# Kernel tuning notes

Hardware: AMD Instinct MI355X
Metric: run time of the kernel (lower is better)

## Reference

```python
import jax, jax.numpy as jnp
import numpy as np

DT = 0.01
T, B, I, H, O = 512, 128, 256, 1024, 256


def setup_inputs() -> dict:
    key = jax.random.key(0)
    ks = jax.random.split(key, 9)
    def xavier(k, out_f, in_f):
        lim = np.sqrt(6.0 / (in_f + out_f)).astype(np.float32)
        return jax.random.uniform(k, (out_f, in_f), jnp.float32, -lim, lim)
    return {
        "x": jax.random.normal(ks[0], (T, B, I), jnp.float32),
        "W_h": xavier(ks[1], H, I + H),                      # HRCell linear, no bias
        "gain": jnp.ones((H,), jnp.float32),
        "omega": jax.random.uniform(ks[2], (H,), jnp.float32, 10.0, 50.0),
        "b_offset": jax.random.uniform(ks[3], (H,), jnp.float32, 1.0, 6.0),
        "W_o": xavier(ks[4], H, H),                          # LICell linear, no bias
        "tau_mem": 20.0 + 5.0 * jax.random.normal(ks[5], (H,), jnp.float32),
        "W_out": xavier(ks[6], O, H),                        # readout Linear
        "b_out": jnp.zeros((O,), jnp.float32),
    }


def reference(x, W_h, gain, omega, b_offset, W_o, tau_mem, W_out, b_out):
    om = jnp.abs(omega)
    om2 = om * om
    b = om2 * 0.005 + jnp.abs(b_offset)          # damping coefficient per unit
    alpha = jnp.exp(-1.0 / jnp.abs(tau_mem))     # leaky-integrator decay
    Bsz = x.shape[1]
    Hd = W_h.shape[0]
    Od = W_out.shape[0]

    def step(carry, x_t):
        hu, hv, ou, acc = carry
        # HRCell: linear on concat(input, hidden_u), then harmonic update
        in_sum = jnp.concatenate([x_t, hu], axis=1) @ W_h.T   # [B, H]
        hv = hv + hu * DT
        hu = hu + in_sum * DT - b * hu * (2.0 * DT) - om2 * hv * DT
        hu = hu * gain                                        # normalize=False path
        # LICell: leaky integrator on projected hidden
        ou = ou * alpha + (hu @ W_o.T) * (1.0 - alpha)
        # readout, summed over time
        acc = acc + ou @ W_out.T + b_out
        return (hu, hv, ou, acc), None

    z = jnp.zeros((Bsz, Hd), x.dtype)
    init = (z, z, z, jnp.zeros((Bsz, Od), x.dtype))
    (hu, hv, ou, acc), _ = jax.lax.scan(step, init, x)
    return acc
```

## Files before the change

### kernel.cpp

```cpp
#include <hip/hip_runtime.h>
#include <math.h>

#define DT 0.01f
constexpr int T = 512, B = 128, I = 256, H = 1024, O = 256;
constexpr int K = I + H;

constexpr size_t OFF_OSUM  = 0;
constexpr size_t OFF_HUH0  = OFF_OSUM + (size_t)B * H;
constexpr size_t OFF_HUL0  = OFF_HUH0 + (size_t)B * H / 2;
constexpr size_t OFF_HUH1  = OFF_HUL0 + (size_t)B * H / 2;
constexpr size_t OFF_HUL1  = OFF_HUH1 + (size_t)B * H / 2;
constexpr size_t OFF_COEF  = OFF_HUL1 + (size_t)B * H / 2;
constexpr size_t OFF_FLAGS = OFF_COEF + 5 * (size_t)H;
constexpr size_t OFF_WHH   = OFF_FLAGS + 8192;
constexpr size_t OFF_WHL   = OFF_WHH + 64 * 40 * 64 * 8 / 2;
constexpr size_t OFF_WOH   = OFF_WHL + 64 * 40 * 64 * 8 / 2;
constexpr size_t OFF_WOL   = OFF_WOH + 64 * 32 * 64 * 8 / 2;

constexpr int SM_WHH  = 0;
constexpr int SM_WHL  = 65536;
constexpr int SM_REDS = 131072;
constexpr int SM_REDP = 139520;
constexpr int SM_BYTES = 147968;

typedef __attribute__((ext_vector_type(8))) short short8v;
typedef __attribute__((ext_vector_type(4))) float f32x4;

static __device__ inline short f2bf(float f) {
    unsigned u = __builtin_bit_cast(unsigned, f);
    u += 0x7fffu + ((u >> 16) & 1u);
    return (short)(u >> 16);
}
static __device__ inline float bf2f(short s) {
    return __builtin_bit_cast(float, ((unsigned)(unsigned short)s) << 16);
}

__global__ __launch_bounds__(256)
void init_kernel(float* __restrict__ ws, const float* __restrict__ omega,
                 const float* __restrict__ b_offset, const float* __restrict__ tau_mem,
                 const float* __restrict__ gain) {
    size_t tid = (size_t)blockIdx.x * blockDim.x + threadIdx.x;
    size_t stride = (size_t)gridDim.x * blockDim.x;
    for (size_t i = tid; i < (size_t)B * H; i += stride) ws[OFF_HUH0 + i] = 0.0f;
    for (size_t i = tid; i < 8192; i += stride) ws[OFF_FLAGS + i] = 0.0f;
    if (tid < H) {
        float om  = fabsf(omega[tid]);
        float om2 = om * om;
        float bb  = om2 * 0.005f + fabsf(b_offset[tid]);
        float al  = expf(-1.0f / fabsf(tau_mem[tid]));
        float g   = gain[tid];
        ws[OFF_COEF + 0 * H + tid] = g * (1.0f - 2.0f * bb * DT);
        ws[OFF_COEF + 1 * H + tid] = g * DT;
        ws[OFF_COEF + 2 * H + tid] = g * om2 * DT;
        ws[OFF_COEF + 3 * H + tid] = al;
        ws[OFF_COEF + 4 * H + tid] = 1.0f - al;
    }
}

template <int NKS, int KD>
__global__ __launch_bounds__(256)
void convert_kernel(const float* __restrict__ W, short* __restrict__ WH,
                    short* __restrict__ WL) {
    int g = blockIdx.x * 256 + threadIdx.x;
    int lane = g & 63;
    int ks = (g >> 6) % NKS;
    int cg = g / (NKS * 64);
    int col = cg * 16 + (lane & 15);
    int k = ks * 32 + ((lane >> 4) << 3);
    const float* src = W + (size_t)col * KD + k;
    short8v hi, lo;
    #pragma unroll
    for (int j = 0; j < 8; ++j) {
        float v = src[j];
        short h = f2bf(v);
        hi[j] = h;
        lo[j] = f2bf(v - bf2f(h));
    }
    *(short8v*)(WH + (size_t)g * 8) = hi;
    *(short8v*)(WL + (size_t)g * 8) = lo;
}

__global__ __launch_bounds__(512)
void rnn_persist(const float* __restrict__ x, float* __restrict__ ws) {
    extern __shared__ char sm[];
    float* redS = (float*)(sm + SM_REDS);
    float* redP = (float*)(sm + SM_REDP);
    __shared__ int role_sm;

    const float* coef = ws + OFF_COEF;
    float* osum_g = ws + OFF_OSUM;
    const short* huhS[2] = {(const short*)(ws + OFF_HUH0), (const short*)(ws + OFF_HUH1)};
    const short* hulS[2] = {(const short*)(ws + OFF_HUL0), (const short*)(ws + OFF_HUL1)};
    unsigned int* huhW[2] = {(unsigned int*)(ws + OFF_HUH0), (unsigned int*)(ws + OFF_HUH1)};
    unsigned int* hulW[2] = {(unsigned int*)(ws + OFF_HUL0), (unsigned int*)(ws + OFF_HUL1)};
    int* flags = (int*)(ws + OFF_FLAGS);
    int* ctr   = flags + 4096;

    const int tid = threadIdx.x;

    if (tid == 0) {
        unsigned xcc_;
        asm volatile("s_getreg_b32 %0, hwreg(HW_REG_XCC_ID)" : "=s"(xcc_));
        int slot = atomicAdd(ctr + (xcc_ & 7), 1);
        role_sm = (int)((xcc_ & 7) * 32 + (slot & 31));
    }
    __syncthreads();
    const int role = role_sm;
    const int xcc = role >> 5;
    const int g   = role & 31;
    const int col0 = g * 32, row0 = xcc * 16;

    const int wid = tid >> 6, lane = tid & 63;
    const int ntile = wid & 1, ksl = wid >> 1;
    const int colgrp = 2 * g + ntile;
    const int rowg = row0 + (lane & 15);
    const int koff = (lane >> 4) << 3;

    {
        const float4* srcH = (const float4*)(ws + OFF_WHH);
        const float4* srcL = (const float4*)(ws + OFF_WHL);
        float4* dH = (float4*)(sm + SM_WHH);
        float4* dL = (float4*)(sm + SM_WHL);
        for (int i = tid; i < 2 * 2048; i += 512) {
            int n = i >> 11, rem = i & 2047;
            dH[i] = srcH[((size_t)(2 * g + n) * 40 + 8) * 64 + rem];
            dL[i] = srcL[((size_t)(2 * g + n) * 40 + 8) * 64 + rem];
        }
    }
    short8v woh[8], wxh[2], wxl[2];
    {
        const short8v* WOHg = (const short8v*)(ws + OFF_WOH) + (size_t)colgrp * 32 * 64 + lane;
        const short8v* WXH  = (const short8v*)(ws + OFF_WHH) + (size_t)colgrp * 40 * 64 + lane;
        const short8v* WXL  = (const short8v*)(ws + OFF_WHL) + (size_t)colgrp * 40 * 64 + lane;
        #pragma unroll
        for (int j = 0; j < 8; ++j) woh[j] = WOHg[(ksl * 8 + j) * 64];
        #pragma unroll
        for (int j = 0; j < 2; ++j) { wxh[j] = WXH[(ksl * 2 + j) * 64]; wxl[j] = WXL[(ksl * 2 + j) * 64]; }
    }
    __syncthreads();

    const short8v* lWHH = (const short8v*)(sm + SM_WHH) + (size_t)ntile * 2048 + lane;
    const short8v* lWHL = (const short8v*)(sm + SM_WHL) + (size_t)ntile * 2048 + lane;

    const int er = tid >> 4;
    const int ec0 = (tid & 15) * 2;
    const int gcol0 = col0 + ec0;
    const size_t erow = (size_t)(row0 + (er & 15));
    float k1a=0,k1b=0,k2a=0,k2b=0,k3a=0,k3b=0, ala=0,alb=0,alma=0,almb=0;
    if (tid < 256) {
        k1a = coef[gcol0];         k1b = coef[gcol0 + 1];
        k2a = coef[H + gcol0];     k2b = coef[H + gcol0 + 1];
        k3a = coef[2 * H + gcol0]; k3b = coef[2 * H + gcol0 + 1];
        ala = coef[3 * H + gcol0]; alb = coef[3 * H + gcol0 + 1];
        alma = coef[4 * H + gcol0]; almb = coef[4 * H + gcol0 + 1];
    }
    float hva=0,hvb=0,oua=0,oub=0,osa=0,osb=0,hua=0,hub=0;

    int* myflag = flags + ((xcc * 32 + g) << 4);
    const size_t rowOffH = (size_t)rowg * H + koff;

    for (int s = 0; s <= T; ++s) {
        const bool last = (s == T);
        f32x4 accS = {0, 0, 0, 0}, accP = {0, 0, 0, 0};

        if (!last) {
            const float* xrow = x + (size_t)s * B * I + (size_t)rowg * I + koff;
            #pragma unroll
            for (int j = 0; j < 2; ++j) {
                float4 a0 = *(const float4*)(xrow + (ksl * 2 + j) * 32);
                float4 a1 = *(const float4*)(xrow + (ksl * 2 + j) * 32 + 4);
                float av[8] = {a0.x,a0.y,a0.z,a0.w,a1.x,a1.y,a1.z,a1.w};
                short8v ah, alv;
                #pragma unroll
                for (int q = 0; q < 8; ++q) {
                    short h = f2bf(av[q]);
                    ah[q] = h;
                    alv[q] = f2bf(av[q] - bf2f(h));
                }
                accS = __builtin_amdgcn_mfma_f32_16x16x32_bf16(ah, wxh[j], accS, 0,0,0);
                accS = __builtin_amdgcn_mfma_f32_16x16x32_bf16(alv, wxh[j], accS, 0,0,0);
                accS = __builtin_amdgcn_mfma_f32_16x16x32_bf16(ah, wxl[j], accS, 0,0,0);
            }
        }

        if (tid < 32) {
            int* pollp = flags + ((xcc * 32 + tid) << 4);
            while (__hip_atomic_load(pollp, __ATOMIC_RELAXED, __HIP_MEMORY_SCOPE_AGENT) < s)
                __builtin_amdgcn_s_sleep(1);
        }
        __syncthreads();
        asm volatile("" ::: "memory");

        const short* hb_ = huhS[s & 1] + rowOffH;
        const short* lb_ = hulS[s & 1] + rowOffH;
        short8v hbuf[8], lbuf[8];
        #pragma unroll
        for (int j = 0; j < 8; ++j) {
            asm volatile("global_load_dwordx4 %0, %1, off sc0" : "=v"(hbuf[j]) : "v"(hb_ + (ksl * 8 + j) * 32));
            asm volatile("global_load_dwordx4 %0, %1, off sc0" : "=v"(lbuf[j]) : "v"(lb_ + (ksl * 8 + j) * 32));
        }
        if (s > 0 && tid < 256) {
            const float* rp = redP + er * 33 + ec0;
            float p0 = (rp[0] + rp[528]) + (rp[1056] + rp[1584]);
            float p1 = (rp[1] + rp[529]) + (rp[1057] + rp[1585]);
            oua = oua * ala + p0 * alma; osa += oua;
            oub = oub * alb + p1 * almb; osb += oub;
        }

        if (!last) {
            asm volatile("s_waitcnt vmcnt(8)");
            __builtin_amdgcn_sched_barrier(0);
            #pragma unroll
            for (int j = 0; j < 4; ++j) {
                short8v ch = lWHH[(ksl * 8 + j) * 64];
                short8v cl = lWHL[(ksl * 8 + j) * 64];
                accS = __builtin_amdgcn_mfma_f32_16x16x32_bf16(hbuf[j], ch, accS, 0,0,0);
                accS = __builtin_amdgcn_mfma_f32_16x16x32_bf16(lbuf[j], ch, accS, 0,0,0);
                accS = __builtin_amdgcn_mfma_f32_16x16x32_bf16(hbuf[j], cl, accS, 0,0,0);
            }
            asm volatile("s_waitcnt vmcnt(0)");
            __builtin_amdgcn_sched_barrier(0);
            #pragma unroll
            for (int j = 4; j < 8; ++j) {
                short8v ch = lWHH[(ksl * 8 + j) * 64];
                short8v cl = lWHL[(ksl * 8 + j) * 64];
                accS = __builtin_amdgcn_mfma_f32_16x16x32_bf16(hbuf[j], ch, accS, 0,0,0);
                accS = __builtin_amdgcn_mfma_f32_16x16x32_bf16(lbuf[j], ch, accS, 0,0,0);
                accS = __builtin_amdgcn_mfma_f32_16x16x32_bf16(hbuf[j], cl, accS, 0,0,0);
            }
            #pragma unroll
            for (int r = 0; r < 4; ++r) {
                int crow = ((lane >> 4) << 2) + r;
                redS[ksl * 528 + crow * 33 + ntile * 16 + (lane & 15)] = accS[r];
            }
            __syncthreads();

            if (tid < 256) {
                const float* rs = redS + er * 33 + ec0;
                float s0 = (rs[0] + rs[528]) + (rs[1056] + rs[1584]);
                float s1 = (rs[1] + rs[529]) + (rs[1057] + rs[1585]);
                float hvn0 = hva + hua * DT;
                float hun0 = k1a * hua + k2a * s0 - k3a * hvn0;
                hva = hvn0; hua = hun0;
                float hvn1 = hvb + hub * DT;
                float hun1 = k1b * hub + k2b * s1 - k3b * hvn1;
                hvb = hvn1; hub = hun1;
                short h0 = f2bf(hun0), h1 = f2bf(hun1);
                short l0 = f2bf(hun0 - bf2f(h0)), l1 = f2bf(hun1 - bf2f(h1));
                unsigned hp = (unsigned)(unsigned short)h0 | ((unsigned)(unsigned short)h1 << 16);
                unsigned lp = (unsigned)(unsigned short)l0 | ((unsigned)(unsigned short)l1 << 16);
                size_t off32 = (erow * H + gcol0) >> 1;
                unsigned int* hp_ = huhW[(s + 1) & 1] + off32;
                unsigned int* lp_ = hulW[(s + 1) & 1] + off32;
                asm volatile("global_store_dword %0, %1, off sc0" :: "v"(hp_), "v"(hp) : "memory");
                asm volatile("global_store_dword %0, %1, off sc0" :: "v"(lp_), "v"(lp) : "memory");
            }
            asm volatile("s_waitcnt vmcnt(0)" ::: "memory");
            __syncthreads();
            if (tid == 0)
                __hip_atomic_store(myflag, s + 1, __ATOMIC_RELAXED, __HIP_MEMORY_SCOPE_AGENT);
        } else {
            asm volatile("s_waitcnt vmcnt(0)");
            __builtin_amdgcn_sched_barrier(0);
            __syncthreads();
        }

        #pragma unroll
        for (int j = 0; j < 8; ++j) {
            accP = __builtin_amdgcn_mfma_f32_16x16x32_bf16(hbuf[j], woh[j], accP, 0,0,0);
            accP = __builtin_amdgcn_mfma_f32_16x16x32_bf16(lbuf[j], woh[j], accP, 0,0,0);
        }
        #pragma unroll
        for (int r = 0; r < 4; ++r) {
            int crow = ((lane >> 4) << 2) + r;
            redP[ksl * 528 + crow * 33 + ntile * 16 + (lane & 15)] = accP[r];
        }
    }

    __syncthreads();
    if (tid < 256) {
        const float* rp = redP + er * 33 + ec0;
        float p0 = (rp[0] + rp[528]) + (rp[1056] + rp[1584]);
        float p1 = (rp[1] + rp[529]) + (rp[1057] + rp[1585]);
        float o0 = oua * ala + p0 * alma; osa += o0;
        float o1 = oub * alb + p1 * almb; osb += o1;
        osum_g[erow * H + gcol0] = osa;
        osum_g[erow * H + gcol0 + 1] = osb;
    }
}

__global__ __launch_bounds__(256)
void readout_kernel(const float* __restrict__ ou_sum, const float* __restrict__ W_out,
                    const float* __restrict__ b_out, float* __restrict__ out) {
    constexpr int KC = 128, BT = 32, CT = 16;
    __shared__ float act[BT][KC + 4];
    __shared__ float w[CT][KC + 4];
    int wg = blockIdx.x;
    int bt = wg & 3, cg = wg >> 2;
    int row0 = bt * BT, col0 = cg * CT;
    int tid = threadIdx.x;
    int c = tid & 15, rr = tid >> 4;

    float4 acc0 = {0, 0, 0, 0}, acc1 = {0, 0, 0, 0};
    for (int kc = 0; kc < H / KC; ++kc) {
        int k0 = kc * KC;
        for (int i = tid; i < BT * (KC / 4); i += 256) {
            int r = i >> 5, c4 = (i & 31) * 4;
            *(float4*)&act[r][c4] = *(const float4*)&ou_sum[(size_t)(row0 + r) * H + k0 + c4];
        }
        for (int i = tid; i < CT * (KC / 4); i += 256) {
            int r = i >> 5, c4 = (i & 31) * 4;
            *(float4*)&w[r][c4] = *(const float4*)&W_out[(size_t)(col0 + r) * H + k0 + c4];
        }
        __syncthreads();
        #pragma unroll
        for (int k4 = 0; k4 < KC / 4; ++k4) {
            float4 a0 = *(const float4*)&act[rr][k4 * 4];
            float4 a1 = *(const float4*)&act[rr + 16][k4 * 4];
            float4 w0 = *(const float4*)&w[c][k4 * 4];
            acc0.x = fmaf(a0.x, w0.x, acc0.x); acc0.y = fmaf(a0.y, w0.y, acc0.y);
            acc0.z = fmaf(a0.z, w0.z, acc0.z); acc0.w = fmaf(a0.w, w0.w, acc0.w);
            acc1.x = fmaf(a1.x, w0.x, acc1.x); acc1.y = fmaf(a1.y, w0.y, acc1.y);
            acc1.z = fmaf(a1.z, w0.z, acc1.z); acc1.w = fmaf(a1.w, w0.w, acc1.w);
        }
        __syncthreads();
    }
    float v0 = (acc0.x + acc0.y) + (acc0.z + acc0.w);
    float v1 = (acc1.x + acc1.y) + (acc1.z + acc1.w);
    int gcol = col0 + c;
    float bo = b_out[gcol] * (float)T;
    out[(size_t)(row0 + rr) * O + gcol] = v0 + bo;
    out[(size_t)(row0 + rr + 16) * O + gcol] = v1 + bo;
}

extern "C" void kernel_launch(void* const* d_in, const int* in_sizes, int n_in,
                              void* d_out, int out_size, void* d_ws, size_t ws_size,
                              hipStream_t stream) {
    const float* x        = (const float*)d_in[0];
    const float* W_h      = (const float*)d_in[1];
    const float* gain     = (const float*)d_in[2];
    const float* omega    = (const float*)d_in[3];
    const float* b_offset = (const float*)d_in[4];
    const float* W_o      = (const float*)d_in[5];
    const float* tau_mem  = (const float*)d_in[6];
    const float* W_out    = (const float*)d_in[7];
    const float* b_out    = (const float*)d_in[8];
    float* ws  = (float*)d_ws;
    float* out = (float*)d_out;

    init_kernel<<<512, 256, 0, stream>>>(ws, omega, b_offset, tau_mem, gain);
    convert_kernel<40, K><<<640, 256, 0, stream>>>(
        W_h, (short*)(ws + OFF_WHH), (short*)(ws + OFF_WHL));
    convert_kernel<32, H><<<512, 256, 0, stream>>>(
        W_o, (short*)(ws + OFF_WOH), (short*)(ws + OFF_WOL));

    rnn_persist<<<256, 512, SM_BYTES, stream>>>(x, ws);

    readout_kernel<<<64, 256, 0, stream>>>(ws + OFF_OSUM, W_out, b_out, out);
}
```

Before: 3.717 ms.

## Unroll recurrence two steps per grid barrier using precomputed squared transition matrix

```diff
diff --git a/kernel.cpp b/kernel.cpp
--- a/kernel.cpp
+++ b/kernel.cpp
@@ -4,23 +4,32 @@
 #define DT 0.01f
 constexpr int T = 512, B = 128, I = 256, H = 1024, O = 256;
 constexpr int K = I + H;
-
-constexpr size_t OFF_OSUM  = 0;
-constexpr size_t OFF_HUH0  = OFF_OSUM + (size_t)B * H;
-constexpr size_t OFF_HUL0  = OFF_HUH0 + (size_t)B * H / 2;
-constexpr size_t OFF_HUH1  = OFF_HUL0 + (size_t)B * H / 2;
-constexpr size_t OFF_HUL1  = OFF_HUH1 + (size_t)B * H / 2;
-constexpr size_t OFF_COEF  = OFF_HUL1 + (size_t)B * H / 2;
-constexpr size_t OFF_FLAGS = OFF_COEF + 5 * (size_t)H;
-constexpr size_t OFF_WHH   = OFF_FLAGS + 8192;
-constexpr size_t OFF_WHL   = OFF_WHH + 64 * 40 * 64 * 8 / 2;
-constexpr size_t OFF_WOH   = OFF_WHL + 64 * 40 * 64 * 8 / 2;
-constexpr size_t OFF_WOL   = OFF_WOH + 64 * 32 * 64 * 8 / 2;
-
-constexpr int SM_WHH  = 0;
-constexpr int SM_WHL  = 65536;
-constexpr int SM_REDS = 131072;
-constexpr int SM_REDP = 139520;
+constexpr int NR = T / 2;
+
+constexpr size_t OFF_OSUM = 0;
+constexpr size_t OFF_MAIN = OFF_OSUM + (size_t)B * H;
+constexpr size_t OFF_WNEG = OFF_MAIN + 262144;
+constexpr size_t OFF_MID  = OFF_WNEG + 262144;
+constexpr size_t OFF_COEF = OFF_MID + 393216;
+constexpr size_t OFF_FLAGS= OFF_COEF + 5 * (size_t)H;
+constexpr size_t OFF_FPH  = OFF_FLAGS + 8256;
+constexpr size_t OFF_FPL  = OFF_FPH + 524288;
+constexpr size_t OFF_FAH  = OFF_FPL + 524288;
+constexpr size_t OFF_FAL  = OFF_FAH + 524288;
+constexpr size_t OFF_FWOH = OFF_FAL + 524288;
+constexpr size_t OFF_FXAH = OFF_FWOH + 524288;
+constexpr size_t OFF_FXAL = OFF_FXAH + 131072;
+constexpr size_t OFF_FXBH = OFF_FXAL + 131072;
+constexpr size_t OFF_FXBL = OFF_FXBH + 131072;
+constexpr size_t OFF_Afp  = OFF_FXBL + 131072;
+constexpr size_t OFF_Pfp  = OFF_Afp + 1048576;
+constexpr size_t OFF_XAfp = OFF_Pfp + 1048576;
+constexpr size_t OFF_XBfp = OFF_XAfp + 262144;
+
+constexpr int SM_PH   = 0;
+constexpr int SM_PL   = 65536;
+constexpr int SM_REDM = 131072;
+constexpr int SM_REDA = 139520;
 constexpr int SM_BYTES = 147968;
 
 typedef __attribute__((ext_vector_type(8))) short short8v;
@@ -41,8 +50,11 @@
                  const float* __restrict__ gain) {
     size_t tid = (size_t)blockIdx.x * blockDim.x + threadIdx.x;
     size_t stride = (size_t)gridDim.x * blockDim.x;
-    for (size_t i = tid; i < (size_t)B * H; i += stride) ws[OFF_HUH0 + i] = 0.0f;
-    for (size_t i = tid; i < 8192; i += stride) ws[OFF_FLAGS + i] = 0.0f;
+    for (size_t i = tid; i < 131072; i += stride) {
+        ws[OFF_MAIN + i] = 0.0f;
+        ws[OFF_WNEG + i] = 0.0f;
+    }
+    for (size_t i = tid; i < 8256; i += stride) ws[OFF_FLAGS + i] = 0.0f;
     if (tid < H) {
         float om  = fabsf(omega[tid]);
         float om2 = om * om;
@@ -55,6 +67,66 @@
         ws[OFF_COEF + 3 * H + tid] = al;
         ws[OFF_COEF + 4 * H + tid] = 1.0f - al;
     }
+}
+
+__global__ __launch_bounds__(256)
+void buildA_kernel(const float* __restrict__ W_h, float* __restrict__ ws) {
+    size_t g = (size_t)blockIdx.x * 256 + threadIdx.x;
+    const float* coef = ws + OFF_COEF;
+    if (g < (size_t)H * H) {
+        int i = (int)(g >> 10), j = (int)(g & 1023);
+        float v = coef[H + i] * W_h[(size_t)i * K + I + j];
+        if (i == j) v += coef[i] - coef[2 * H + i] * DT;
+        ws[OFF_Afp + g] = v;
+    }
+    if (g < (size_t)H * I) {
+        int i = (int)(g >> 8), j = (int)(g & 255);
+        ws[OFF_XBfp + g] = coef[H + i] * W_h[(size_t)i * K + j];
+    }
+}
+
+__global__ __launch_bounds__(256)
+void gemm_transB(const float* __restrict__ X, const float* __restrict__ Bsrc,
+                 float* __restrict__ C, int N, int Kd, int bstride) {
+    constexpr int KC = 128;
+    __shared__ float act[32][KC + 4];
+    __shared__ float w[16][KC + 4];
+    int bt = blockIdx.x & 31, cgi = blockIdx.x >> 5;
+    int row0 = bt * 32, col0 = cgi * 16;
+    int tid = threadIdx.x;
+    int c = tid & 15, rr = tid >> 4;
+    float4 acc0 = {0,0,0,0}, acc1 = {0,0,0,0};
+    for (int kc = 0; kc < Kd / KC; ++kc) {
+        int k0 = kc * KC;
+        for (int i = tid; i < 32 * (KC / 4); i += 256) {
+            int r = i >> 5, c4 = (i & 31) * 4;
+            *(float4*)&act[r][c4] = *(const float4*)&X[(size_t)(row0 + r) * Kd + k0 + c4];
+        }
+        for (int i = tid; i < 16 * KC; i += 256) {
+            int j = i & 15, kk = i >> 4;
+            w[j][kk] = Bsrc[(size_t)(k0 + kk) * bstride + col0 + j];
+        }
+        __syncthreads();
+        #pragma unroll
+        for (int k4 = 0; k4 < KC / 4; ++k4) {
+            float4 a0 = *(const float4*)&act[rr][k4 * 4];
+            float4 a1 = *(const float4*)&act[rr + 16][k4 * 4];
+            float4 w0 = *(const float4*)&w[c][k4 * 4];
+            acc0.x = fmaf(a0.x, w0.x, acc0.x); acc0.y = fmaf(a0.y, w0.y, acc0.y);
+            acc0.z = fmaf(a0.z, w0.z, acc0.z); acc0.w = fmaf(a0.w, w0.w, acc0.w);
+            acc1.x = fmaf(a1.x, w0.x, acc1.x); acc1.y = fmaf(a1.y, w0.y, acc1.y);
+            acc1.z = fmaf(a1.z, w0.z, acc1.z); acc1.w = fmaf(a1.w, w0.w, acc1.w);
+        }
+        __syncthreads();
+    }
+    C[(size_t)(row0 + rr) * N + col0 + c] = (acc0.x + acc0.y) + (acc0.z + acc0.w);
+    C[(size_t)(row0 + rr + 16) * N + col0 + c] = (acc1.x + acc1.y) + (acc1.z + acc1.w);
+}
+
+__global__ __launch_bounds__(256)
+void fixP_kernel(float* __restrict__ ws) {
+    int i = blockIdx.x * 256 + threadIdx.x;
+    if (i < H) ws[OFF_Pfp + (size_t)i * H + i] -= DT * ws[OFF_COEF + 2 * H + i];
 }
 
 template <int NKS, int KD>
@@ -79,25 +151,38 @@
     *(short8v*)(WH + (size_t)g * 8) = hi;
     *(short8v*)(WL + (size_t)g * 8) = lo;
 }
+template <int NKS, int KD>
+__global__ __launch_bounds__(256)
+void convertH_kernel(const float* __restrict__ W, short* __restrict__ WH) {
+    int g = blockIdx.x * 256 + threadIdx.x;
+    int lane = g & 63;
+    int ks = (g >> 6) % NKS;
+    int cg = g / (NKS * 64);
+    int col = cg * 16 + (lane & 15);
+    int k = ks * 32 + ((lane >> 4) << 3);
+    const float* src = W + (size_t)col * KD + k;
+    short8v hi;
+    #pragma unroll
+    for (int j = 0; j < 8; ++j) hi[j] = f2bf(src[j]);
+    *(short8v*)(WH + (size_t)g * 8) = hi;
+}
 
 __global__ __launch_bounds__(512)
 void rnn_persist(const float* __restrict__ x, float* __restrict__ ws) {
     extern __shared__ char sm[];
-    float* redS = (float*)(sm + SM_REDS);
-    float* redP = (float*)(sm + SM_REDP);
+    float* redM = (float*)(sm + SM_REDM);
+    float* redA = (float*)(sm + SM_REDA);
     __shared__ int role_sm;
 
     const float* coef = ws + OFF_COEF;
     float* osum_g = ws + OFF_OSUM;
-    const short* huhS[2] = {(const short*)(ws + OFF_HUH0), (const short*)(ws + OFF_HUH1)};
-    const short* hulS[2] = {(const short*)(ws + OFF_HUL0), (const short*)(ws + OFF_HUL1)};
-    unsigned int* huhW[2] = {(unsigned int*)(ws + OFF_HUH0), (unsigned int*)(ws + OFF_HUH1)};
-    unsigned int* hulW[2] = {(unsigned int*)(ws + OFF_HUL0), (unsigned int*)(ws + OFF_HUL1)};
+    short* MAIN = (short*)(ws + OFF_MAIN);
+    short* WNEG = (short*)(ws + OFF_WNEG);
+    short* MID  = (short*)(ws + OFF_MID);
     int* flags = (int*)(ws + OFF_FLAGS);
-    int* ctr   = flags + 4096;
+    int* ctr   = flags + 8192;
 
     const int tid = threadIdx.x;
-
     if (tid == 0) {
         unsigned xcc_;
         asm volatile("s_getreg_b32 %0, hwreg(HW_REG_XCC_ID)" : "=s"(xcc_));
@@ -106,184 +191,275 @@
     }
     __syncthreads();
     const int role = role_sm;
-    const int xcc = role >> 5;
-    const int g   = role & 31;
+    const int xcc = role >> 5, g = role & 31;
     const int col0 = g * 32, row0 = xcc * 16;
 
     const int wid = tid >> 6, lane = tid & 63;
     const int ntile = wid & 1, ksl = wid >> 1;
-    const int colgrp = 2 * g + ntile;
+    const int cg = 2 * g + ntile;
     const int rowg = row0 + (lane & 15);
     const int koff = (lane >> 4) << 3;
+    const size_t rowOff = (size_t)rowg * H + koff;
 
     {
-        const float4* srcH = (const float4*)(ws + OFF_WHH);
-        const float4* srcL = (const float4*)(ws + OFF_WHL);
-        float4* dH = (float4*)(sm + SM_WHH);
-        float4* dL = (float4*)(sm + SM_WHL);
+        const float4* sH = (const float4*)(ws + OFF_FPH);
+        const float4* sL = (const float4*)(ws + OFF_FPL);
+        float4* dH = (float4*)(sm + SM_PH);
+        float4* dL = (float4*)(sm + SM_PL);
         for (int i = tid; i < 2 * 2048; i += 512) {
             int n = i >> 11, rem = i & 2047;
-            dH[i] = srcH[((size_t)(2 * g + n) * 40 + 8) * 64 + rem];
-            dL[i] = srcL[((size_t)(2 * g + n) * 40 + 8) * 64 + rem];
-        }
-    }
-    short8v woh[8], wxh[2], wxl[2];
+            dH[i] = sH[(size_t)(2 * g + n) * 2048 + rem];
+            dL[i] = sL[(size_t)(2 * g + n) * 2048 + rem];
+        }
+    }
+    short8v ahi[8], alo[8];
     {
-        const short8v* WOHg = (const short8v*)(ws + OFF_WOH) + (size_t)colgrp * 32 * 64 + lane;
-        const short8v* WXH  = (const short8v*)(ws + OFF_WHH) + (size_t)colgrp * 40 * 64 + lane;
-        const short8v* WXL  = (const short8v*)(ws + OFF_WHL) + (size_t)colgrp * 40 * 64 + lane;
+        const short8v* AH = (const short8v*)(ws + OFF_FAH) + (size_t)cg * 32 * 64 + lane;
+        const short8v* AL = (const short8v*)(ws + OFF_FAL) + (size_t)cg * 32 * 64 + lane;
         #pragma unroll
-        for (int j = 0; j < 8; ++j) woh[j] = WOHg[(ksl * 8 + j) * 64];
-        #pragma unroll
-        for (int j = 0; j < 2; ++j) { wxh[j] = WXH[(ksl * 2 + j) * 64]; wxl[j] = WXL[(ksl * 2 + j) * 64]; }
+        for (int j = 0; j < 8; ++j) { ahi[j] = AH[(ksl * 8 + j) * 64]; alo[j] = AL[(ksl * 8 + j) * 64]; }
     }
     __syncthreads();
 
-    const short8v* lWHH = (const short8v*)(sm + SM_WHH) + (size_t)ntile * 2048 + lane;
-    const short8v* lWHL = (const short8v*)(sm + SM_WHL) + (size_t)ntile * 2048 + lane;
+    const short8v* lPH = (const short8v*)(sm + SM_PH) + (size_t)ntile * 2048 + lane;
+    const short8v* lPL = (const short8v*)(sm + SM_PL) + (size_t)ntile * 2048 + lane;
+    const short8v* FWO = (const short8v*)(ws + OFF_FWOH) + (size_t)cg * 32 * 64 + lane;
+    const short8v* FXAH = (const short8v*)(ws + OFF_FXAH) + (size_t)cg * 8 * 64 + lane;
+    const short8v* FXAL = (const short8v*)(ws + OFF_FXAL) + (size_t)cg * 8 * 64 + lane;
+    const short8v* FXBH = (const short8v*)(ws + OFF_FXBH) + (size_t)cg * 8 * 64 + lane;
+    const short8v* FXBL = (const short8v*)(ws + OFF_FXBL) + (size_t)cg * 8 * 64 + lane;
 
     const int er = tid >> 4;
     const int ec0 = (tid & 15) * 2;
     const int gcol0 = col0 + ec0;
     const size_t erow = (size_t)(row0 + (er & 15));
-    float k1a=0,k1b=0,k2a=0,k2b=0,k3a=0,k3b=0, ala=0,alb=0,alma=0,almb=0;
+    float k3a=0,k3b=0, ala=0,alb=0, alma=0,almb=0;
     if (tid < 256) {
-        k1a = coef[gcol0];         k1b = coef[gcol0 + 1];
-        k2a = coef[H + gcol0];     k2b = coef[H + gcol0 + 1];
         k3a = coef[2 * H + gcol0]; k3b = coef[2 * H + gcol0 + 1];
         ala = coef[3 * H + gcol0]; alb = coef[3 * H + gcol0 + 1];
         alma = coef[4 * H + gcol0]; almb = coef[4 * H + gcol0 + 1];
     }
-    float hva=0,hvb=0,oua=0,oub=0,osa=0,osb=0,hua=0,hub=0;
+    float hua=0, hub=0, hva=0, hvb=0, oua=0, oub=0, osa=0, osb=0;
 
     int* myflag = flags + ((xcc * 32 + g) << 4);
-    const size_t rowOffH = (size_t)rowg * H + koff;
-
-    for (int s = 0; s <= T; ++s) {
-        const bool last = (s == T);
-        f32x4 accS = {0, 0, 0, 0}, accP = {0, 0, 0, 0};
-
-        if (!last) {
-            const float* xrow = x + (size_t)s * B * I + (size_t)rowg * I + koff;
-            #pragma unroll
-            for (int j = 0; j < 2; ++j) {
-                float4 a0 = *(const float4*)(xrow + (ksl * 2 + j) * 32);
-                float4 a1 = *(const float4*)(xrow + (ksl * 2 + j) * 32 + 4);
+    short8v hbuf[8], lbuf[8];
+
+    for (int r = 0; r <= NR; ++r) {
+        const bool lastR = (r == NR);
+        f32x4 accM = {0,0,0,0}, accA = {0,0,0,0};
+
+        if (!lastR) {
+            const float* x0row = x + (size_t)(2 * r) * B * I + (size_t)rowg * I + koff;
+            const float* x1row = x0row + B * I;
+            #pragma unroll
+            for (int jj = 0; jj < 2; ++jj) {
+                int ksx = ksl * 2 + jj;
+                float4 a0 = *(const float4*)(x0row + ksx * 32);
+                float4 a1 = *(const float4*)(x0row + ksx * 32 + 4);
+                float4 b0 = *(const float4*)(x1row + ksx * 32);
+                float4 b1 = *(const float4*)(x1row + ksx * 32 + 4);
                 float av[8] = {a0.x,a0.y,a0.z,a0.w,a1.x,a1.y,a1.z,a1.w};
-                short8v ah, alv;
+                float bv[8] = {b0.x,b0.y,b0.z,b0.w,b1.x,b1.y,b1.z,b1.w};
+                short8v xh0, xl0, xh1, xl1;
                 #pragma unroll
                 for (int q = 0; q < 8; ++q) {
-                    short h = f2bf(av[q]);
-                    ah[q] = h;
-                    alv[q] = f2bf(av[q] - bf2f(h));
-                }
-                accS = __builtin_amdgcn_mfma_f32_16x16x32_bf16(ah, wxh[j], accS, 0,0,0);
-                accS = __builtin_amdgcn_mfma_f32_16x16x32_bf16(alv, wxh[j], accS, 0,0,0);
-                accS = __builtin_amdgcn_mfma_f32_16x16x32_bf16(ah, wxl[j], accS, 0,0,0);
+                    short h0 = f2bf(av[q]); xh0[q] = h0; xl0[q] = f2bf(av[q] - bf2f(h0));
+                    short h1 = f2bf(bv[q]); xh1[q] = h1; xl1[q] = f2bf(bv[q] - bf2f(h1));
+                }
+                short8v XaH = FXAH[ksx * 64], XaL = FXAL[ksx * 64];
+                short8v XbH = FXBH[ksx * 64], XbL = FXBL[ksx * 64];
+                accM = __builtin_amdgcn_mfma_f32_16x16x32_bf16(xh0, XaH, accM, 0,0,0);
+                accM = __builtin_amdgcn_mfma_f32_16x16x32_bf16(xl0, XaH, accM, 0,0,0);
+                accM = __builtin_amdgcn_mfma_f32_16x16x32_bf16(xh0, XaL, accM, 0,0,0);
+                accM = __builtin_amdgcn_mfma_f32_16x16x32_bf16(xh1, XbH, accM, 0,0,0);
+                accM = __builtin_amdgcn_mfma_f32_16x16x32_bf16(xl1, XbH, accM, 0,0,0);
+                accM = __builtin_amdgcn_mfma_f32_16x16x32_bf16(xh1, XbL, accM, 0,0,0);
+                accA = __builtin_amdgcn_mfma_f32_16x16x32_bf16(xh0, XbH, accA, 0,0,0);
+                accA = __builtin_amdgcn_mfma_f32_16x16x32_bf16(xl0, XbH, accA, 0,0,0);
+                accA = __builtin_amdgcn_mfma_f32_16x16x32_bf16(xh0, XbL, accA, 0,0,0);
             }
         }
 
         if (tid < 32) {
             int* pollp = flags + ((xcc * 32 + tid) << 4);
-            while (__hip_atomic_load(pollp, __ATOMIC_RELAXED, __HIP_MEMORY_SCOPE_AGENT) < s)
+            while (__hip_atomic_load(pollp, __ATOMIC_RELAXED, __HIP_MEMORY_SCOPE_AGENT) < r)
                 __builtin_amdgcn_s_sleep(1);
         }
         __syncthreads();
         asm volatile("" ::: "memory");
 
-        const short* hb_ = huhS[s & 1] + rowOffH;
-        const short* lb_ = hulS[s & 1] + rowOffH;
-        short8v hbuf[8], lbuf[8];
+        const short* hb = MAIN + (size_t)(r & 1) * 262144 + rowOff;
+        const short* lb = hb + 131072;
+        __builtin_amdgcn_sched_barrier(0);
         #pragma unroll
         for (int j = 0; j < 8; ++j) {
-            asm volatile("global_load_dwordx4 %0, %1, off sc0" : "=v"(hbuf[j]) : "v"(hb_ + (ksl * 8 + j) * 32));
-            asm volatile("global_load_dwordx4 %0, %1, off sc0" : "=v"(lbuf[j]) : "v"(lb_ + (ksl * 8 + j) * 32));
-        }
-        if (s > 0 && tid < 256) {
-            const float* rp = redP + er * 33 + ec0;
-            float p0 = (rp[0] + rp[528]) + (rp[1056] + rp[1584]);
-            float p1 = (rp[1] + rp[529]) + (rp[1057] + rp[1585]);
-            oua = oua * ala + p0 * alma; osa += oua;
-            oub = oub * alb + p1 * almb; osb += oub;
-        }
-
-        if (!last) {
+            asm volatile("global_load_dwordx4 %0, %1, off sc0" : "=v"(hbuf[j]) : "v"(hb + (ksl * 8 + j) * 32));
+            asm volatile("global_load_dwordx4 %0, %1, off sc0" : "=v"(lbuf[j]) : "v"(lb + (ksl * 8 + j) * 32));
+        }
+        if (!lastR) {
+            const short* wb = WNEG + (size_t)(r & 1) * 262144 + rowOff;
+            const short* vb = wb + 131072;
+            short8v wbh[8], wbl[8];
+            #pragma unroll
+            for (int j = 0; j < 8; ++j) {
+                asm volatile("global_load_dwordx4 %0, %1, off sc0" : "=v"(wbh[j]) : "v"(wb + (ksl * 8 + j) * 32));
+                asm volatile("global_load_dwordx4 %0, %1, off sc0" : "=v"(wbl[j]) : "v"(vb + (ksl * 8 + j) * 32));
+            }
+            asm volatile("s_waitcnt vmcnt(24)");
+            __builtin_amdgcn_sched_barrier(0);
+            #pragma unroll
+            for (int j = 0; j < 4; ++j) {
+                short8v ph = lPH[(ksl * 8 + j) * 64], pl = lPL[(ksl * 8 + j) * 64];
+                accM = __builtin_amdgcn_mfma_f32_16x16x32_bf16(hbuf[j], ph, accM, 0,0,0);
+                accM = __builtin_amdgcn_mfma_f32_16x16x32_bf16(lbuf[j], ph, accM, 0,0,0);
+                accM = __builtin_amdgcn_mfma_f32_16x16x32_bf16(hbuf[j], pl, accM, 0,0,0);
+                accA = __builtin_amdgcn_mfma_f32_16x16x32_bf16(hbuf[j], ahi[j], accA, 0,0,0);
+                accA = __builtin_amdgcn_mfma_f32_16x16x32_bf16(lbuf[j], ahi[j], accA, 0,0,0);
+                accA = __builtin_amdgcn_mfma_f32_16x16x32_bf16(hbuf[j], alo[j], accA, 0,0,0);
+            }
+            asm volatile("s_waitcnt vmcnt(16)");
+            __builtin_amdgcn_sched_barrier(0);
+            #pragma unroll
+            for (int j = 4; j < 8; ++j) {
+                short8v ph = lPH[(ksl * 8 + j) * 64], pl = lPL[(ksl * 8 + j) * 64];
+                accM = __builtin_amdgcn_mfma_f32_16x16x32_bf16(hbuf[j], ph, accM, 0,0,0);
+                accM = __builtin_amdgcn_mfma_f32_16x16x32_bf16(lbuf[j], ph, accM, 0,0,0);
+                accM = __builtin_amdgcn_mfma_f32_16x16x32_bf16(hbuf[j], pl, accM, 0,0,0);
+                accA = __builtin_amdgcn_mfma_f32_16x16x32_bf16(hbuf[j], ahi[j], accA, 0,0,0);
+                accA = __builtin_amdgcn_mfma_f32_16x16x32_bf16(lbuf[j], ahi[j], accA, 0,0,0);
+                accA = __builtin_amdgcn_mfma_f32_16x16x32_bf16(hbuf[j], alo[j], accA, 0,0,0);
+            }
             asm volatile("s_waitcnt vmcnt(8)");
             __builtin_amdgcn_sched_barrier(0);
             #pragma unroll
             for (int j = 0; j < 4; ++j) {
-                short8v ch = lWHH[(ksl * 8 + j) * 64];
-                short8v cl = lWHL[(ksl * 8 + j) * 64];
-                accS = __builtin_amdgcn_mfma_f32_16x16x32_bf16(hbuf[j], ch, accS, 0,0,0);
-                accS = __builtin_amdgcn_mfma_f32_16x16x32_bf16(lbuf[j], ch, accS, 0,0,0);
-                accS = __builtin_amdgcn_mfma_f32_16x16x32_bf16(hbuf[j], cl, accS, 0,0,0);
+                accM = __builtin_amdgcn_mfma_f32_16x16x32_bf16(wbh[j], ahi[j], accM, 0,0,0);
+                accM = __builtin_amdgcn_mfma_f32_16x16x32_bf16(wbl[j], ahi[j], accM, 0,0,0);
+                accM = __builtin_amdgcn_mfma_f32_16x16x32_bf16(wbh[j], alo[j], accM, 0,0,0);
             }
             asm volatile("s_waitcnt vmcnt(0)");
             __builtin_amdgcn_sched_barrier(0);
             #pragma unroll
             for (int j = 4; j < 8; ++j) {
-                short8v ch = lWHH[(ksl * 8 + j) * 64];
-                short8v cl = lWHL[(ksl * 8 + j) * 64];
-                accS = __builtin_amdgcn_mfma_f32_16x16x32_bf16(hbuf[j], ch, accS, 0,0,0);
-                accS = __builtin_amdgcn_mfma_f32_16x16x32_bf16(lbuf[j], ch, accS, 0,0,0);
-                accS = __builtin_amdgcn_mfma_f32_16x16x32_bf16(hbuf[j], cl, accS, 0,0,0);
-            }
-            #pragma unroll
-            for (int r = 0; r < 4; ++r) {
-                int crow = ((lane >> 4) << 2) + r;
-                redS[ksl * 528 + crow * 33 + ntile * 16 + (lane & 15)] = accS[r];
-            }
-            __syncthreads();
-
+                accM = __builtin_amdgcn_mfma_f32_16x16x32_bf16(wbh[j], ahi[j], accM, 0,0,0);
+                accM = __builtin_amdgcn_mfma_f32_16x16x32_bf16(wbl[j], ahi[j], accM, 0,0,0);
+                accM = __builtin_amdgcn_mfma_f32_16x16x32_bf16(wbh[j], alo[j], accM, 0,0,0);
+            }
+            #pragma unroll
+            for (int rr = 0; rr < 4; ++rr) {
+                int crow = ((lane >> 4) << 2) + rr;
+                redM[ksl * 528 + crow * 33 + ntile * 16 + (lane & 15)] = accM[rr];
+                redA[ksl * 528 + crow * 33 + ntile * 16 + (lane & 15)] = accA[rr];
+            }
+        }
+        __syncthreads();
+
+        if (!lastR) {
             if (tid < 256) {
-                const float* rs = redS + er * 33 + ec0;
-                float s0 = (rs[0] + rs[528]) + (rs[1056] + rs[1584]);
-                float s1 = (rs[1] + rs[529]) + (rs[1057] + rs[1585]);
-                float hvn0 = hva + hua * DT;
-                float hun0 = k1a * hua + k2a * s0 - k3a * hvn0;
-                hva = hvn0; hua = hun0;
-                float hvn1 = hvb + hub * DT;
-                float hun1 = k1b * hub + k2b * s1 - k3b * hvn1;
-                hvb = hvn1; hub = hun1;
-                short h0 = f2bf(hun0), h1 = f2bf(hun1);
-                short l0 = f2bf(hun0 - bf2f(h0)), l1 = f2bf(hun1 - bf2f(h1));
-                unsigned hp = (unsigned)(unsigned short)h0 | ((unsigned)(unsigned short)h1 << 16);
-                unsigned lp = (unsigned)(unsigned short)l0 | ((unsigned)(unsigned short)l1 << 16);
+                int base = er * 33 + ec0;
+                float m0 = (redM[base] + redM[528 + base]) + (redM[1056 + base] + redM[1584 + base]);
+                float m1 = (redM[base + 1] + redM[528 + base + 1]) + (redM[1056 + base + 1] + redM[1584 + base + 1]);
+                float a0 = (redA[base] + redA[528 + base]) + (redA[1056 + base] + redA[1584 + base]);
+                float a1 = (redA[base + 1] + redA[528 + base + 1]) + (redA[1056 + base + 1] + redA[1584 + base + 1]);
+                float wna = -k3a * hva, wnb = -k3b * hvb;
+                float hu1a = a0 + wna, hu1b = a1 + wnb;
+                float hu2a = m0 + wna, hu2b = m1 + wnb;
+                float hv2a = hva + DT * (hua + hu1a);
+                float hv2b = hvb + DT * (hub + hu1b);
+                hua = hu2a; hub = hu2b; hva = hv2a; hvb = hv2b;
                 size_t off32 = (erow * H + gcol0) >> 1;
-                unsigned int* hp_ = huhW[(s + 1) & 1] + off32;
-                unsigned int* lp_ = hulW[(s + 1) & 1] + off32;
-                asm volatile("global_store_dword %0, %1, off sc0" :: "v"(hp_), "v"(hp) : "memory");
-                asm volatile("global_store_dword %0, %1, off sc0" :: "v"(lp_), "v"(lp) : "memory");
+                {
+                    short h0 = f2bf(hu1a), h1 = f2bf(hu1b);
+                    short l0 = f2bf(hu1a - bf2f(h0)), l1 = f2bf(hu1b - bf2f(h1));
+                    unsigned hp = (unsigned)(unsigned short)h0 | ((unsigned)(unsigned short)h1 << 16);
+                    unsigned lp = (unsigned)(unsigned short)l0 | ((unsigned)(unsigned short)l1 << 16);
+                    unsigned* hd = (unsigned*)(MID + (size_t)(r % 3) * 262144) + off32;
+                    unsigned* ld = (unsigned*)(MID + (size_t)(r % 3) * 262144 + 131072) + off32;
+                    asm volatile("global_store_dword %0, %1, off sc0" :: "v"(hd), "v"(hp) : "memory");
+                    asm volatile("global_store_dword %0, %1, off sc0" :: "v"(ld), "v"(lp) : "memory");
+                }
+                {
+                    short h0 = f2bf(hu2a), h1 = f2bf(hu2b);
+                    short l0 = f2bf(hu2a - bf2f(h0)), l1 = f2bf(hu2b - bf2f(h1));
+                    unsigned hp = (unsigned)(unsigned short)h0 | ((unsigned)(unsigned short)h1 << 16);
+                    unsigned lp = (unsigned)(unsigned short)l0 | ((unsigned)(unsigned short)l1 << 16);
+                    unsigned* hd = (unsigned*)(MAIN + (size_t)((r + 1) & 1) * 262144) + off32;
+                    unsigned* ld = (unsigned*)(MAIN + (size_t)((r + 1) & 1) * 262144 + 131072) + off32;
+                    asm volatile("global_store_dword %0, %1, off sc0" :: "v"(hd), "v"(hp) : "memory");
+                    asm volatile("global_store_dword %0, %1, off sc0" :: "v"(ld), "v"(lp) : "memory");
+                }
+                {
+                    float wa = -k3a * hv2a, wb_ = -k3b * hv2b;
+                    short h0 = f2bf(wa), h1 = f2bf(wb_);
+                    short l0 = f2bf(wa - bf2f(h0)), l1 = f2bf(wb_ - bf2f(h1));
+                    unsigned hp = (unsigned)(unsigned short)h0 | ((unsigned)(unsigned short)h1 << 16);
+                    unsigned lp = (unsigned)(unsigned short)l0 | ((unsigned)(unsigned short)l1 << 16);
+                    unsigned* hd = (unsigned*)(WNEG + (size_t)((r + 1) & 1) * 262144) + off32;
+                    unsigned* ld = (unsigned*)(WNEG + (size_t)((r + 1) & 1) * 262144 + 131072) + off32;
+                    asm volatile("global_store_dword %0, %1, off sc0" :: "v"(hd), "v"(hp) : "memory");
+                    asm volatile("global_store_dword %0, %1, off sc0" :: "v"(ld), "v"(lp) : "memory");
+                }
             }
             asm volatile("s_waitcnt vmcnt(0)" ::: "memory");
             __syncthreads();
             if (tid == 0)
-                __hip_atomic_store(myflag, s + 1, __ATOMIC_RELAXED, __HIP_MEMORY_SCOPE_AGENT);
-        } else {
-            asm volatile("s_waitcnt vmcnt(0)");
-            __builtin_amdgcn_sched_barrier(0);
+                __hip_atomic_store(myflag, r + 1, __ATOMIC_RELAXED, __HIP_MEMORY_SCOPE_AGENT);
+        }
+
+        {
+            if (lastR) { asm volatile("s_waitcnt vmcnt(0)"); __builtin_amdgcn_sched_barrier(0); }
+            f32x4 q0 = {0,0,0,0};
+            #pragma unroll
+            for (int j = 0; j < 8; ++j) {
+                short8v wo = FWO[(ksl * 8 + j) * 64];
+                q0 = __builtin_amdgcn_mfma_f32_16x16x32_bf16(hbuf[j], wo, q0, 0,0,0);
+                q0 = __builtin_amdgcn_mfma_f32_16x16x32_bf16(lbuf[j], wo, q0, 0,0,0);
+            }
+            f32x4 q1 = {0,0,0,0};
+            if (r >= 1) {
+                const short* mh = MID + (size_t)((r - 1) % 3) * 262144 + rowOff;
+                const short* ml = mh + 131072;
+                short8v mhb[8], mlb[8];
+                #pragma unroll
+                for (int j = 0; j < 8; ++j) {
+                    asm volatile("global_load_dwordx4 %0, %1, off sc0" : "=v"(mhb[j]) : "v"(mh + (ksl * 8 + j) * 32));
+                    asm volatile("global_load_dwordx4 %0, %1, off sc0" : "=v"(mlb[j]) : "v"(ml + (ksl * 8 + j) * 32));
+                }
+                asm volatile("s_waitcnt vmcnt(0)");
+                __builtin_amdgcn_sched_barrier(0);
+                #pragma unroll
+                for (int j = 0; j < 8; ++j) {
+                    short8v wo = FWO[(ksl * 8 + j) * 64];
+                    q1 = __builtin_amdgcn_mfma_f32_16x16x32_bf16(mhb[j], wo, q1, 0,0,0);
+                    q1 = __builtin_amdgcn_mfma_f32_16x16x32_bf16(mlb[j], wo, q1, 0,0,0);
+                }
+            }
+            #pragma unroll
+            for (int rr = 0; rr < 4; ++rr) {
+                int crow = ((lane >> 4) << 2) + rr;
+                redM[ksl * 528 + crow * 33 + ntile * 16 + (lane & 15)] = q0[rr];
+                redA[ksl * 528 + crow * 33 + ntile * 16 + (lane & 15)] = q1[rr];
+            }
             __syncthreads();
-        }
-
-        #pragma unroll
-        for (int j = 0; j < 8; ++j) {
-            accP = __builtin_amdgcn_mfma_f32_16x16x32_bf16(hbuf[j], woh[j], accP, 0,0,0);
-            accP = __builtin_amdgcn_mfma_f32_16x16x32_bf16(lbuf[j], woh[j], accP, 0,0,0);
-        }
-        #pragma unroll
-        for (int r = 0; r < 4; ++r) {
-            int crow = ((lane >> 4) << 2) + r;
-            redP[ksl * 528 + crow * 33 + ntile * 16 + (lane & 15)] = accP[r];
-        }
-    }
-
-    __syncthreads();
+            if (tid < 256) {
+                int base = er * 33 + ec0;
+                if (r >= 1) {
+                    float v0 = (redA[base] + redA[528 + base]) + (redA[1056 + base] + redA[1584 + base]);
+                    float v1 = (redA[base + 1] + redA[528 + base + 1]) + (redA[1056 + base + 1] + redA[1584 + base + 1]);
+                    oua = ala * oua + alma * v0; osa += oua;
+                    oub = alb * oub + almb * v1; osb += oub;
+                }
+                {
+                    float v0 = (redM[base] + redM[528 + base]) + (redM[1056 + base] + redM[1584 + base]);
+                    float v1 = (redM[base + 1] + redM[528 + base + 1]) + (redM[1056 + base + 1] + redM[1584 + base + 1]);
+                    oua = ala * oua + alma * v0; osa += oua;
+                    oub = alb * oub + almb * v1; osb += oub;
+                }
+            }
+        }
+    }
+
     if (tid < 256) {
-        const float* rp = redP + er * 33 + ec0;
-        float p0 = (rp[0] + rp[528]) + (rp[1056] + rp[1584]);
-        float p1 = (rp[1] + rp[529]) + (rp[1057] + rp[1585]);
-        float o0 = oua * ala + p0 * alma; osa += o0;
-        float o1 = oub * alb + p1 * almb; osb += o1;
         osum_g[erow * H + gcol0] = osa;
         osum_g[erow * H + gcol0 + 1] = osb;
     }
@@ -300,8 +476,7 @@
     int row0 = bt * BT, col0 = cg * CT;
     int tid = threadIdx.x;
     int c = tid & 15, rr = tid >> 4;
-
-    float4 acc0 = {0, 0, 0, 0}, acc1 = {0, 0, 0, 0};
+    float4 acc0 = {0,0,0,0}, acc1 = {0,0,0,0};
     for (int kc = 0; kc < H / KC; ++kc) {
         int k0 = kc * KC;
         for (int i = tid; i < BT * (KC / 4); i += 256) {
@@ -349,10 +524,15 @@
     float* out = (float*)d_out;
 
     init_kernel<<<512, 256, 0, stream>>>(ws, omega, b_offset, tau_mem, gain);
-    convert_kernel<40, K><<<640, 256, 0, stream>>>(
-        W_h, (short*)(ws + OFF_WHH), (short*)(ws + OFF_WHL));
-    convert_kernel<32, H><<<512, 256, 0, stream>>>(
-        W_o, (short*)(ws + OFF_WOH), (short*)(ws + OFF_WOL));
+    buildA_kernel<<<4096, 256, 0, stream>>>(W_h, ws);
+    gemm_transB<<<2048, 256, 0, stream>>>(ws + OFF_Afp, ws + OFF_Afp, ws + OFF_Pfp, 1024, 1024, 1024);
+    fixP_kernel<<<4, 256, 0, stream>>>(ws);
+    gemm_transB<<<512, 256, 0, stream>>>(ws + OFF_Afp, ws + OFF_XBfp, ws + OFF_XAfp, 256, 1024, 256);
+    convert_kernel<32, 1024><<<512, 256, 0, stream>>>(ws + OFF_Pfp, (short*)(ws + OFF_FPH), (short*)(ws + OFF_FPL));
+    convert_kernel<32, 1024><<<512, 256, 0, stream>>>(ws + OFF_Afp, (short*)(ws + OFF_FAH), (short*)(ws + OFF_FAL));
+    convertH_kernel<32, 1024><<<512, 256, 0, stream>>>(W_o, (short*)(ws + OFF_FWOH));
+    convert_kernel<8, 256><<<128, 256, 0, stream>>>(ws + OFF_XAfp, (short*)(ws + OFF_FXAH), (short*)(ws + OFF_FXAL));
+    convert_kernel<8, 256><<<128, 256, 0, stream>>>(ws + OFF_XBfp, (short*)(ws + OFF_FXBH), (short*)(ws + OFF_FXBL));
 
     rnn_persist<<<256, 512, SM_BYTES, stream>>>(x, ws);
 
```

Result: slower. 5.074 ms (+36.5%).
